# Kernel tuning notes

Hardware: AMD Instinct MI355X
Metric: run time of the kernel (lower is better)

The kernel has to match this reference:

```python
import jax, jax.numpy as jnp
import numpy as np

DIM = 2048
N_HEADS = 16
HEAD_DIM = DIM // N_HEADS
ROPE_BASE = 10000.0


def _rope_cos_sin(seq_len, head_dim, dtype):
    inv_freq = 1.0 / (ROPE_BASE ** (jnp.arange(0, head_dim, 2, dtype=jnp.float32) / head_dim))
    t = jnp.arange(seq_len, dtype=jnp.float32)
    freqs = jnp.einsum('s,d->sd', t, inv_freq)          # (S, hd/2)
    emb = jnp.concatenate([freqs, freqs], axis=-1)       # (S, hd)
    return jnp.cos(emb).astype(dtype), jnp.sin(emb).astype(dtype)


def _rotate_half(x):
    x1, x2 = jnp.split(x, 2, axis=-1)
    return jnp.concatenate([-x2, x1], axis=-1)


def _apply_rope(x, cos, sin):
    # x: (B, H, S, hd); cos/sin: (S, hd)
    return x * cos[None, None] + _rotate_half(x) * sin[None, None]


def setup_inputs() -> dict:
    key = jax.random.key(0)
    ks = jax.random.split(key, 5)
    B, S = 2, 2048
    scale = 1.0 / np.sqrt(DIM)
    return {
        'x': jax.random.normal(ks[0], (B, S, DIM), dtype=jnp.float32),
        'Wq': jax.random.normal(ks[1], (DIM, DIM), dtype=jnp.float32) * scale,
        'Wk': jax.random.normal(ks[2], (DIM, DIM), dtype=jnp.float32) * scale,
        'Wv': jax.random.normal(ks[3], (DIM, DIM), dtype=jnp.float32) * scale,
        'Wo': jax.random.normal(ks[4], (DIM, DIM), dtype=jnp.float32) * scale,
    }


def reference(x, Wq, Wk, Wv, Wo):
    B, S, _ = x.shape
    scale = HEAD_DIM ** -0.5

    def proj(W):
        # torch Linear: x @ W.T ; reshape to (B, H, S, hd)
        return (x @ W.T).reshape(B, S, N_HEADS, HEAD_DIM).transpose(0, 2, 1, 3)

    q, k, v = proj(Wq), proj(Wk), proj(Wv)
    cos, sin = _rope_cos_sin(S, HEAD_DIM, x.dtype)
    q = _apply_rope(q, cos, sin)
    k = _apply_rope(k, cos, sin)

    scores = jnp.einsum('bhqd,bhkd->bhqk', q, k) * scale  # (B,H,S,S)
    causal = jnp.triu(jnp.ones((S, S), dtype=bool), k=1)
    scores = jnp.where(causal[None, None], -jnp.inf, scores)
    attn = jax.nn.softmax(scores.astype(jnp.float32), axis=-1).astype(q.dtype)
    out = jnp.einsum('bhqk,bhkd->bhqd', attn, v)          # (B,H,S,hd)
    out = out.transpose(0, 2, 1, 3).reshape(B, S, DIM)
    return out @ Wo.T
```

## Files before the change

### kernel.cpp

```cpp
#include <hip/hip_runtime.h>


#define SEQ 2048
#define DMODEL 2048
#define NH 16
#define HD 128

typedef __attribute__((ext_vector_type(8))) short bf16x8;
typedef __attribute__((ext_vector_type(4))) float f32x4;

__device__ __forceinline__ unsigned short f2bf(float f) {
  unsigned int u = __float_as_uint(f);
  u += 0x7fffu + ((u >> 16) & 1u);
  return (unsigned short)(u >> 16);
}

__device__ __forceinline__ void g2l16(const void* g, void* l) {
  __builtin_amdgcn_global_load_lds((const __attribute__((address_space(1))) void*)g,
                                   (__attribute__((address_space(3))) void*)l,
                                   16, 0, 0);
}

__device__ __forceinline__ f32x4 mfma16(bf16x8 a, bf16x8 b, f32x4 c) {
  return __builtin_amdgcn_mfma_f32_16x16x32_bf16(a, b, c, 0, 0, 0);
}

template <int CTRL>
__device__ __forceinline__ float dpp_ror(float v) {
  return __int_as_float(__builtin_amdgcn_mov_dpp(__float_as_int(v), CTRL, 0xf, 0xf, false));
}
__device__ __forceinline__ float red_max16(float v) {
  v = fmaxf(v, dpp_ror<0x128>(v));
  v = fmaxf(v, dpp_ror<0x124>(v));
  v = fmaxf(v, dpp_ror<0x122>(v));
  v = fmaxf(v, dpp_ror<0x121>(v));
  return v;
}
__device__ __forceinline__ float red_sum16(float v) {
  v += dpp_ror<0x128>(v);
  v += dpp_ror<0x124>(v);
  v += dpp_ror<0x122>(v);
  v += dpp_ror<0x121>(v);
  return v;
}

__global__ __launch_bounds__(256) void cvt_all(const float* __restrict__ x,
                                               const float* __restrict__ wq,
                                               const float* __restrict__ wk,
                                               const float* __restrict__ wv,
                                               const float* __restrict__ wo,
                                               unsigned short* __restrict__ dst0,
                                               float2* __restrict__ rtab) {
  const int b = blockIdx.x;
  if (b >= 24576) {
    const int idx = (b - 24576) * 256 + threadIdx.x;
    const int s = idx >> 6, d = idx & 63;
    float sn, cs;
    sincosf((float)s * exp2f(-0.20762050593046f * (float)d), &sn, &cs);
    rtab[idx] = make_float2(cs, sn);
    return;
  }
  const float* src;
  unsigned short* dst;
  int idx, r = -1;
  if (b < 8192) {
    src = x; dst = dst0; idx = b * 256 + threadIdx.x;
  } else {
    r = (b - 8192) >> 12;
    src = (r == 0) ? wq : (r == 1) ? wk : (r == 2) ? wv : wo;
    dst = dst0 + (size_t)2 * SEQ * DMODEL + (size_t)r * DMODEL * DMODEL;
    idx = ((b - 8192) & 4095) * 256 + threadIdx.x;
  }
  const float4 v = ((const float4*)src)[idx];
  ushort4 o;
  o.x = f2bf(v.x); o.y = f2bf(v.y); o.z = f2bf(v.z); o.w = f2bf(v.w);
  int widx = idx;
  if (r == 0 || r == 1) {
    const int row = idx >> 9, col = idx & 511;
    const int o_ = row & 127;
    const int e = (((o_ >> 4) & 3) << 5) | (((o_ >> 6) & 1) << 4) | (o_ & 15);
    widx = (((row & ~127) | e) << 9) | col;
  }
  ((ushort4*)dst)[widx] = o;
}

template <int MODE>
__global__ __launch_bounds__(512, 2) void gemm_pipe(
    const unsigned short* __restrict__ A,
    const unsigned short* __restrict__ B,
    unsigned short* __restrict__ obf,
    float* __restrict__ of32,
    const float2* __restrict__ rtab) {
  constexpr int BN = (MODE == 0) ? 192 : 128;
  constexpr int NTW = BN / 32;
  constexpr int TILE = (256 + BN) * 64;
  constexpr int NU = 32 + BN / 8;
  constexpr int UPW = NU / 8;
  __shared__ unsigned short lds[2 * TILE];
  const int nb = blockIdx.x, mb = blockIdx.y;
  const int M0 = mb * 256;
  const int t = threadIdx.x;
  const int w = t >> 6, lane = t & 63, l15 = lane & 15, quad = lane >> 4;
  const int g = lane >> 3, j = lane & 7;
  const int wm = w >> 1, wn = w & 1;

  const unsigned short* Abase = A + (size_t)M0 * DMODEL;
  const unsigned short* Bbase = B + (size_t)nb * BN * DMODEL;

  f32x4 acc[4][NTW] = {};

  auto stage = [&](int buf, int k0, int i0, int i1) {
#pragma unroll
    for (int i = i0; i < i1; ++i) {
      const int u = w * UPW + i;
      if (u < 32) {
        g2l16(Abase + (size_t)(u * 8 + g) * DMODEL + k0 + ((j ^ g) << 3),
              &lds[buf * TILE + u * 512]);
      } else {
        g2l16(Bbase + (size_t)((u - 32) * 8 + g) * DMODEL + k0 + ((j ^ g) << 3),
              &lds[buf * TILE + 16384 + (u - 32) * 512]);
      }
    }
  };

  auto comp = [&](int buf, int kc) {
    const int c = kc * 4 + quad;
    const unsigned short* As_ = &lds[buf * TILE];
    const unsigned short* Bs_ = &lds[buf * TILE + 16384];
    bf16x8 af[4], bv[NTW];
#pragma unroll
    for (int mt = 0; mt < 4; ++mt) {
      const int m = wm * 64 + mt * 16 + l15;
      af[mt] = *(const bf16x8*)&As_[m * 64 + ((c ^ (m & 7)) << 3)];
    }
#pragma unroll
    for (int nt = 0; nt < NTW; ++nt) {
      const int n = wn * (BN / 2) + nt * 16 + l15;
      bv[nt] = *(const bf16x8*)&Bs_[n * 64 + ((c ^ (n & 7)) << 3)];
    }
#pragma unroll
    for (int nt = 0; nt < NTW; ++nt)
#pragma unroll
      for (int mt = 0; mt < 4; ++mt)
        acc[mt][nt] = mfma16(af[mt], bv[nt], acc[mt][nt]);
  };

  stage(0, 0, 0, UPW);
  asm volatile("s_waitcnt vmcnt(0)\n\ts_barrier" ::: "memory");

  int buf = 0;
  for (int tt = 0; tt < 32; ++tt) {
    const bool ps = (tt < 31);
    if (ps) stage(buf ^ 1, tt * 64 + 64, 0, UPW / 2);
    comp(buf, 0);
    if (ps) stage(buf ^ 1, tt * 64 + 64, UPW / 2, UPW);
    comp(buf, 1);
    if (ps) {
      asm volatile("s_waitcnt vmcnt(0)\n\ts_barrier" ::: "memory");
      buf ^= 1;
    }
  }

  if (MODE == 0) {
    const size_t NX = (size_t)2 * SEQ * DMODEL;
#pragma unroll
    for (int pp = 0; pp < NTW / 2; ++pp) {
      const int colb = nb * BN + wn * (BN / 2) + pp * 32;
      const int z = colb >> 11;
      const int zc = colb & 2047;
      const int h = zc >> 7;
      const int e0 = zc & 127;
      if (z < 2) {
        const float qscale = (z == 0) ? 0.1275174356f : 1.0f;
        unsigned short* O = obf + (size_t)z * NX;
        const int rt = (e0 >> 5) * 16 + l15;
#pragma unroll
        for (int mt = 0; mt < 4; ++mt)
#pragma unroll
          for (int reg = 0; reg < 4; ++reg) {
            const int m = M0 + wm * 64 + mt * 16 + quad * 4 + reg;
            const int bb = m >> 11, s = m & 2047;
            unsigned short* ob = O + ((size_t)(bb * NH + h) * SEQ + s) * HD;
            const float2 cs = rtab[s * 64 + rt];
            const float x1 = acc[mt][2 * pp][reg], x2 = acc[mt][2 * pp + 1][reg];
            ob[e0 + l15] = f2bf((x1 * cs.x - x2 * cs.y) * qscale);
            ob[e0 + 16 + l15] = f2bf((x2 * cs.x + x1 * cs.y) * qscale);
          }
      } else {
        unsigned short* Vb0 = obf + 2 * NX + (size_t)h * HD * SEQ;
#pragma unroll
        for (int q2 = 0; q2 < 2; ++q2) {
          const int d = e0 + q2 * 16 + l15;
#pragma unroll
          for (int mt = 0; mt < 4; ++mt)
#pragma unroll
            for (int reg = 0; reg < 4; ++reg) {
              const int m = M0 + wm * 64 + mt * 16 + quad * 4 + reg;
              const int bb = m >> 11, s = m & 2047;
              unsigned short* ob = Vb0 + (size_t)bb * NH * HD * SEQ;
              ob[(size_t)d * SEQ + s] = f2bf(acc[mt][2 * pp + q2][reg]);
            }
        }
      }
    }
  } else {
#pragma unroll
    for (int mt = 0; mt < 4; ++mt)
#pragma unroll
      for (int reg = 0; reg < 4; ++reg) {
        const int m = M0 + wm * 64 + mt * 16 + quad * 4 + reg;
#pragma unroll
        for (int nt = 0; nt < NTW; ++nt)
          of32[(size_t)m * DMODEL + nb * BN + wn * (BN / 2) + nt * 16 + l15] =
              acc[mt][nt][reg];
      }
  }
}

__global__ __launch_bounds__(256) void attn_kernel(const unsigned short* __restrict__ Q,
                                                   const unsigned short* __restrict__ K,
                                                   const unsigned short* __restrict__ Vt,
                                                   unsigned short* __restrict__ Oa) {
  __shared__ unsigned short Ks[2][64 * 128];
  __shared__ unsigned short Vs[2][128 * 64];
  __shared__ unsigned short Ps[4][1024];
  const int gid = blockIdx.x;
  const int bh = gid & 31;
  const int pr = gid >> 5;
  const unsigned short* Qb = Q + (size_t)bh * SEQ * HD;
  const unsigned short* Kb = K + (size_t)bh * SEQ * HD;
  const unsigned short* Vb = Vt + (size_t)bh * HD * SEQ;
  const int t = threadIdx.x;
  const int w = t >> 6, lane = t & 63, l15 = lane & 15, quad = lane >> 4;
  const int l7 = lane & 7;
  const int b = bh >> 4, h = bh & 15;
  const int uA = w * 64 + lane;

  auto stage = [&](int sb, int kt) {
    const unsigned short* Kt = Kb + (size_t)(kt * 64) * HD;
    const unsigned short* Vtk = Vb + kt * 64;
#pragma unroll
    for (int i = 0; i < 4; ++i) {
      const int u = i * 256 + uA;
      const int key = u >> 4, cs = u & 15;
      g2l16(Kt + (size_t)key * HD + ((cs ^ (key & 7)) << 3),
            &Ks[sb][(i * 256 + w * 64) * 8]);
    }
#pragma unroll
    for (int i = 0; i < 4; ++i) {
      const int u = i * 256 + uA;
      const int d = u >> 3, cs = u & 7;
      g2l16(Vtk + (size_t)d * SEQ + ((cs ^ (d & 7)) << 3),
            &Vs[sb][(i * 256 + w * 64) * 8]);
    }
  };

  for (int half = 0; half < 2; ++half) {
    const int qt = half ? 31 - pr : pr;

    bf16x8 qf[4];
#pragma unroll
    for (int ch = 0; ch < 4; ++ch)
      qf[ch] = *(const bf16x8*)(Qb + (size_t)(qt * 64 + w * 16 + l15) * HD +
                                ch * 32 + quad * 8);

    f32x4 o[8] = {};
    float mrow[4], lrow[4];
#pragma unroll
    for (int reg = 0; reg < 4; ++reg) { mrow[reg] = -1e30f; lrow[reg] = 0.f; }

    stage(0, 0);
    asm volatile("s_waitcnt vmcnt(0)\n\ts_barrier" ::: "memory");
    int buf = 0;

    for (int kt = 0; kt <= qt; ++kt) {
      if (kt < qt) stage(buf ^ 1, kt + 1);

      const bool diag = (kt == qt);
      const int ntm = diag ? w : 3;
      f32x4 s[4] = {};
      __builtin_amdgcn_s_setprio(1);
#pragma unroll
      for (int ch = 0; ch < 4; ++ch) {
        const int c = ch * 4 + quad;
#pragma unroll
        for (int nt = 0; nt < 4; ++nt) {
          if (nt <= ntm) {
            const int n = nt * 16 + l15;
            const bf16x8 bv = *(const bf16x8*)&Ks[buf][n * 128 + ((c ^ l7) << 3)];
            s[nt] = mfma16(qf[ch], bv, s[nt]);
          }
        }
      }
      __builtin_amdgcn_s_setprio(0);

      if (diag) {
#pragma unroll
        for (int nt = 0; nt < 4; ++nt)
#pragma unroll
          for (int reg = 0; reg < 4; ++reg) {
            const int rr = w * 16 + quad * 4 + reg;
            const int cc = nt * 16 + l15;
            if (cc > rr) s[nt][reg] = -1e30f;
          }
      }

#pragma unroll
      for (int reg = 0; reg < 4; ++reg) {
        float vmax = s[0][reg];
#pragma unroll
        for (int nt = 1; nt < 4; ++nt) vmax = fmaxf(vmax, s[nt][reg]);
        vmax = red_max16(vmax);
        const float mo = mrow[reg];
        float mn = mo;
        if (!__all(vmax <= mo + 8.0f)) {
          mn = fmaxf(mo, vmax);
          const float alpha = exp2f(mo - mn);
          mrow[reg] = mn;
          lrow[reg] *= alpha;
#pragma unroll
          for (int nt = 0; nt < 8; ++nt) o[nt][reg] *= alpha;
        }
        float rs = 0.f;
#pragma unroll
        for (int nt = 0; nt < 4; ++nt) {
          const float p_ = exp2f(s[nt][reg] - mn);
          s[nt][reg] = p_;
          rs += p_;
        }
        rs = red_sum16(rs);
        lrow[reg] += rs;
      }

      unsigned short* Pw = Ps[w];
#pragma unroll
      for (int nt = 0; nt < 4; ++nt)
#pragma unroll
        for (int reg = 0; reg < 4; ++reg) {
          const int key = nt * 16 + l15;
          Pw[(key >> 3) * 128 + (quad * 4 + reg) * 8 + (key & 7)] = f2bf(s[nt][reg]);
        }

      __builtin_amdgcn_s_setprio(1);
#pragma unroll
      for (int ch2 = 0; ch2 < 2; ++ch2) {
        const int c = ch2 * 4 + quad;
        const bf16x8 pa = *(const bf16x8*)&Pw[c * 128 + l15 * 8];
#pragma unroll
        for (int nt = 0; nt < 8; ++nt) {
          const int d = nt * 16 + l15;
          const bf16x8 vv = *(const bf16x8*)&Vs[buf][d * 64 + ((c ^ l7) << 3)];
          o[nt] = mfma16(pa, vv, o[nt]);
        }
      }
      __builtin_amdgcn_s_setprio(0);

      asm volatile("s_waitcnt vmcnt(0)\n\ts_barrier" ::: "memory");
      buf ^= 1;
    }

#pragma unroll
    for (int reg = 0; reg < 4; ++reg) {
      const int sq = qt * 64 + w * 16 + quad * 4 + reg;
      const float inv_l = 1.0f / lrow[reg];
      unsigned short* ob = Oa + (size_t)(b * SEQ + sq) * DMODEL + h * HD;
#pragma unroll
      for (int nt = 0; nt < 8; ++nt) ob[nt * 16 + l15] = f2bf(o[nt][reg] * inv_l);
    }
  }
}

extern "C" void kernel_launch(void* const* d_in, const int* in_sizes, int n_in,
                              void* d_out, int out_size, void* d_ws, size_t ws_size,
                              hipStream_t stream) {
  const float* x = (const float*)d_in[0];
  const float* Wq = (const float*)d_in[1];
  const float* Wk = (const float*)d_in[2];
  const float* Wv = (const float*)d_in[3];
  const float* Wo = (const float*)d_in[4];
  float* out = (float*)d_out;

  const size_t NX = (size_t)2 * SEQ * DMODEL;
  const size_t NW = (size_t)DMODEL * DMODEL;
  unsigned short* ws = (unsigned short*)d_ws;
  unsigned short* xb = ws;
  unsigned short* wqb = xb + NX;
  unsigned short* wkb = wqb + NW;
  unsigned short* wvb = wkb + NW;
  unsigned short* wob = wvb + NW;
  unsigned short* qb = wob + NW;
  unsigned short* kb = qb + NX;
  unsigned short* vb = kb + NX;
  unsigned short* ab = vb + NX;
  float2* rtab = (float2*)(ab + NX);

  cvt_all<<<25088, 256, 0, stream>>>(x, Wq, Wk, Wv, Wo, ws, rtab);
  gemm_pipe<0><<<dim3(32, 16), 512, 0, stream>>>(xb, wqb, qb, nullptr, rtab);
  attn_kernel<<<512, 256, 0, stream>>>(qb, kb, vb, ab);
  gemm_pipe<1><<<dim3(16, 16), 512, 0, stream>>>(ab, wob, nullptr, out, nullptr);
}
```

Baseline: 356.7 us.

## Use 128-row query tiles with 8 waves per attention block and packed P stores

The attention kernel now gives each 512-thread block a 128-query tile instead of processing two 64-query tiles in turn, so every staged K/V tile is shared by twice as many waves. Work is ordered longest-first, and waves whose rows are fully masked skip the tile. P is written to LDS as packed bf16 pairs through a swizzled layout, and the V projection writes keys in a permuted order so the PV step can read P directly. The cost is a larger block, possible imbalance between waves on diagonal tiles, and more intricate indexing that could hide correctness bugs.

```diff
diff --git a/kernel.cpp b/kernel.cpp
--- a/kernel.cpp
+++ b/kernel.cpp
@@ -197,8 +197,10 @@
             for (int reg = 0; reg < 4; ++reg) {
               const int m = M0 + wm * 64 + mt * 16 + quad * 4 + reg;
               const int bb = m >> 11, s = m & 2047;
+              const int spos = (s & ~63) |
+                               ((mt >> 1) * 32 + quad * 8 + reg * 2 + (mt & 1));
               unsigned short* ob = Vb0 + (size_t)bb * NH * HD * SEQ;
-              ob[(size_t)d * SEQ + s] = f2bf(acc[mt][2 * pp + q2][reg]);
+              ob[(size_t)d * SEQ + spos] = f2bf(acc[mt][2 * pp + q2][reg]);
             }
         }
       }
@@ -217,67 +219,64 @@
   }
 }
 
-__global__ __launch_bounds__(256) void attn_kernel(const unsigned short* __restrict__ Q,
-                                                   const unsigned short* __restrict__ K,
-                                                   const unsigned short* __restrict__ Vt,
-                                                   unsigned short* __restrict__ Oa) {
+__global__ __launch_bounds__(512, 4) void attn_kernel(const unsigned short* __restrict__ Q,
+                                                      const unsigned short* __restrict__ K,
+                                                      const unsigned short* __restrict__ Vt,
+                                                      unsigned short* __restrict__ Oa) {
   __shared__ unsigned short Ks[2][64 * 128];
   __shared__ unsigned short Vs[2][128 * 64];
-  __shared__ unsigned short Ps[4][1024];
+  __shared__ unsigned short Ps[8][1024];
   const int gid = blockIdx.x;
   const int bh = gid & 31;
-  const int pr = gid >> 5;
+  const int qt = 15 - (gid >> 5);
   const unsigned short* Qb = Q + (size_t)bh * SEQ * HD;
   const unsigned short* Kb = K + (size_t)bh * SEQ * HD;
   const unsigned short* Vb = Vt + (size_t)bh * HD * SEQ;
   const int t = threadIdx.x;
   const int w = t >> 6, lane = t & 63, l15 = lane & 15, quad = lane >> 4;
-  const int l7 = lane & 7;
   const int b = bh >> 4, h = bh & 15;
-  const int uA = w * 64 + lane;
 
   auto stage = [&](int sb, int kt) {
     const unsigned short* Kt = Kb + (size_t)(kt * 64) * HD;
     const unsigned short* Vtk = Vb + kt * 64;
 #pragma unroll
-    for (int i = 0; i < 4; ++i) {
-      const int u = i * 256 + uA;
+    for (int i = 0; i < 2; ++i) {
+      const int u = i * 512 + t;
       const int key = u >> 4, cs = u & 15;
       g2l16(Kt + (size_t)key * HD + ((cs ^ (key & 7)) << 3),
-            &Ks[sb][(i * 256 + w * 64) * 8]);
-    }
-#pragma unroll
-    for (int i = 0; i < 4; ++i) {
-      const int u = i * 256 + uA;
+            &Ks[sb][(i * 512 + w * 64) * 8]);
+    }
+#pragma unroll
+    for (int i = 0; i < 2; ++i) {
+      const int u = i * 512 + t;
       const int d = u >> 3, cs = u & 7;
       g2l16(Vtk + (size_t)d * SEQ + ((cs ^ (d & 7)) << 3),
-            &Vs[sb][(i * 256 + w * 64) * 8]);
+            &Vs[sb][(i * 512 + w * 64) * 8]);
     }
   };
 
-  for (int half = 0; half < 2; ++half) {
-    const int qt = half ? 31 - pr : pr;
-
-    bf16x8 qf[4];
-#pragma unroll
-    for (int ch = 0; ch < 4; ++ch)
-      qf[ch] = *(const bf16x8*)(Qb + (size_t)(qt * 64 + w * 16 + l15) * HD +
-                                ch * 32 + quad * 8);
-
-    f32x4 o[8] = {};
-    float mrow[4], lrow[4];
-#pragma unroll
-    for (int reg = 0; reg < 4; ++reg) { mrow[reg] = -1e30f; lrow[reg] = 0.f; }
-
-    stage(0, 0);
-    asm volatile("s_waitcnt vmcnt(0)\n\ts_barrier" ::: "memory");
-    int buf = 0;
-
-    for (int kt = 0; kt <= qt; ++kt) {
-      if (kt < qt) stage(buf ^ 1, kt + 1);
-
-      const bool diag = (kt == qt);
-      const int ntm = diag ? w : 3;
+  bf16x8 qf[4];
+#pragma unroll
+  for (int ch = 0; ch < 4; ++ch)
+    qf[ch] = *(const bf16x8*)(Qb + (size_t)(qt * 128 + w * 16 + l15) * HD +
+                              ch * 32 + quad * 8);
+
+  f32x4 o[8] = {};
+  float mrow[4], lrow[4];
+#pragma unroll
+  for (int reg = 0; reg < 4; ++reg) { mrow[reg] = -1e30f; lrow[reg] = 0.f; }
+
+  const int ktmax = 2 * qt + 1;
+  stage(0, 0);
+  asm volatile("s_waitcnt vmcnt(0)\n\ts_barrier" ::: "memory");
+  int buf = 0;
+
+  for (int kt = 0; kt <= ktmax; ++kt) {
+    if (kt < ktmax) stage(buf ^ 1, kt + 1);
+
+    const int ntm_raw = (qt * 128 + w * 16 + 15 - kt * 64) >> 4;
+    const int ntm = ntm_raw > 3 ? 3 : ntm_raw;
+    if (ntm >= 0) {
       f32x4 s[4] = {};
       __builtin_amdgcn_s_setprio(1);
 #pragma unroll
@@ -287,29 +286,27 @@
         for (int nt = 0; nt < 4; ++nt) {
           if (nt <= ntm) {
             const int n = nt * 16 + l15;
-            const bf16x8 bv = *(const bf16x8*)&Ks[buf][n * 128 + ((c ^ l7) << 3)];
+            const bf16x8 bv = *(const bf16x8*)&Ks[buf][n * 128 + ((c ^ (n & 7)) << 3)];
             s[nt] = mfma16(qf[ch], bv, s[nt]);
           }
         }
       }
       __builtin_amdgcn_s_setprio(0);
 
-      if (diag) {
+      if (kt >= 2 * qt) {
 #pragma unroll
         for (int nt = 0; nt < 4; ++nt)
 #pragma unroll
           for (int reg = 0; reg < 4; ++reg) {
-            const int rr = w * 16 + quad * 4 + reg;
-            const int cc = nt * 16 + l15;
+            const int rr = qt * 128 + w * 16 + quad * 4 + reg;
+            const int cc = kt * 64 + nt * 16 + l15;
             if (cc > rr) s[nt][reg] = -1e30f;
           }
       }
 
 #pragma unroll
       for (int reg = 0; reg < 4; ++reg) {
-        float vmax = s[0][reg];
-#pragma unroll
-        for (int nt = 1; nt < 4; ++nt) vmax = fmaxf(vmax, s[nt][reg]);
+        float vmax = fmaxf(fmaxf(s[0][reg], s[1][reg]), fmaxf(s[2][reg], s[3][reg]));
         vmax = red_max16(vmax);
         const float mo = mrow[reg];
         float mn = mo;
@@ -334,39 +331,50 @@
 
       unsigned short* Pw = Ps[w];
 #pragma unroll
-      for (int nt = 0; nt < 4; ++nt)
+      for (int np = 0; np < 2; ++np)
 #pragma unroll
         for (int reg = 0; reg < 4; ++reg) {
-          const int key = nt * 16 + l15;
-          Pw[(key >> 3) * 128 + (quad * 4 + reg) * 8 + (key & 7)] = f2bf(s[nt][reg]);
-        }
-
+          unsigned int u;
+          asm("v_cvt_pk_bf16_f32 %0, %1, %2"
+              : "=v"(u)
+              : "v"(s[np * 2][reg]), "v"(s[np * 2 + 1][reg]));
+          const int r = quad * 4 + reg;
+          const int ph = ((np ^ (quad & 1)) * 4 + (l15 >> 2) + r) & 7;
+          *(unsigned int*)&Pw[r * 64 + ph * 8 + (l15 & 3) * 2] = u;
+        }
+      asm volatile("" ::: "memory");
+
+      const int ch2max = (ntm >= 2) ? 1 : 0;
       __builtin_amdgcn_s_setprio(1);
 #pragma unroll
       for (int ch2 = 0; ch2 < 2; ++ch2) {
-        const int c = ch2 * 4 + quad;
-        const bf16x8 pa = *(const bf16x8*)&Pw[c * 128 + l15 * 8];
-#pragma unroll
-        for (int nt = 0; nt < 8; ++nt) {
-          const int d = nt * 16 + l15;
-          const bf16x8 vv = *(const bf16x8*)&Vs[buf][d * 64 + ((c ^ l7) << 3)];
-          o[nt] = mfma16(pa, vv, o[nt]);
+        if (ch2 <= ch2max) {
+          const int pnp = ch2 ^ ((l15 >> 2) & 1);
+          const int ph = (pnp * 4 + quad + l15) & 7;
+          const bf16x8 pa = *(const bf16x8*)&Pw[l15 * 64 + ph * 8];
+          const int c = ch2 * 4 + quad;
+#pragma unroll
+          for (int nt = 0; nt < 8; ++nt) {
+            const int d = nt * 16 + l15;
+            const bf16x8 vv = *(const bf16x8*)&Vs[buf][d * 64 + ((c ^ (d & 7)) << 3)];
+            o[nt] = mfma16(pa, vv, o[nt]);
+          }
         }
       }
       __builtin_amdgcn_s_setprio(0);
-
-      asm volatile("s_waitcnt vmcnt(0)\n\ts_barrier" ::: "memory");
-      buf ^= 1;
-    }
-
-#pragma unroll
-    for (int reg = 0; reg < 4; ++reg) {
-      const int sq = qt * 64 + w * 16 + quad * 4 + reg;
-      const float inv_l = 1.0f / lrow[reg];
-      unsigned short* ob = Oa + (size_t)(b * SEQ + sq) * DMODEL + h * HD;
-#pragma unroll
-      for (int nt = 0; nt < 8; ++nt) ob[nt * 16 + l15] = f2bf(o[nt][reg] * inv_l);
-    }
+    }
+
+    asm volatile("s_waitcnt vmcnt(0)\n\ts_barrier" ::: "memory");
+    buf ^= 1;
+  }
+
+#pragma unroll
+  for (int reg = 0; reg < 4; ++reg) {
+    const int sq = qt * 128 + w * 16 + quad * 4 + reg;
+    const float inv_l = 1.0f / lrow[reg];
+    unsigned short* ob = Oa + (size_t)(b * SEQ + sq) * DMODEL + h * HD;
+#pragma unroll
+    for (int nt = 0; nt < 8; ++nt) ob[nt * 16 + l15] = f2bf(o[nt][reg] * inv_l);
   }
 }
 
@@ -396,6 +404,6 @@
 
   cvt_all<<<25088, 256, 0, stream>>>(x, Wq, Wk, Wv, Wo, ws, rtab);
   gemm_pipe<0><<<dim3(32, 16), 512, 0, stream>>>(xb, wqb, qb, nullptr, rtab);
-  attn_kernel<<<512, 256, 0, stream>>>(qb, kb, vb, ab);
+  attn_kernel<<<512, 512, 0, stream>>>(qb, kb, vb, ab);
   gemm_pipe<1><<<dim3(16, 16), 512, 0, stream>>>(ab, wob, nullptr, out, nullptr);
 }
```

After: 362.7 us. About the same (+1.7%).

## Permute V key order to pack P with paired bf16 stores and skip masked PV chunk

Applied to the files above, without the earlier changes.

The V projection epilogue now writes keys within each 64-block in a permuted order that matches the MFMA accumulator layout. The attention kernel can then convert pairs of P values with v_cvt_pk_bf16_f32 and store them as 32-bit swizzled words instead of scalar 16-bit stores. On the diagonal tile it skips the second PV chunk when it is fully masked. This reduces LDS store count and conversion work in the softmax-to-PV handoff, but the permutation has to match exactly between the producer and the consumer.

```diff
diff --git a/kernel.cpp b/kernel.cpp
--- a/kernel.cpp
+++ b/kernel.cpp
@@ -197,8 +197,10 @@
             for (int reg = 0; reg < 4; ++reg) {
               const int m = M0 + wm * 64 + mt * 16 + quad * 4 + reg;
               const int bb = m >> 11, s = m & 2047;
+              const int spos = (s & ~63) |
+                               ((mt >> 1) * 32 + quad * 8 + reg * 2 + (mt & 1));
               unsigned short* ob = Vb0 + (size_t)bb * NH * HD * SEQ;
-              ob[(size_t)d * SEQ + s] = f2bf(acc[mt][2 * pp + q2][reg]);
+              ob[(size_t)d * SEQ + spos] = f2bf(acc[mt][2 * pp + q2][reg]);
             }
         }
       }
@@ -232,7 +234,6 @@
   const unsigned short* Vb = Vt + (size_t)bh * HD * SEQ;
   const int t = threadIdx.x;
   const int w = t >> 6, lane = t & 63, l15 = lane & 15, quad = lane >> 4;
-  const int l7 = lane & 7;
   const int b = bh >> 4, h = bh & 15;
   const int uA = w * 64 + lane;
 
@@ -278,6 +279,7 @@
 
       const bool diag = (kt == qt);
       const int ntm = diag ? w : 3;
+
       f32x4 s[4] = {};
       __builtin_amdgcn_s_setprio(1);
 #pragma unroll
@@ -287,7 +289,7 @@
         for (int nt = 0; nt < 4; ++nt) {
           if (nt <= ntm) {
             const int n = nt * 16 + l15;
-            const bf16x8 bv = *(const bf16x8*)&Ks[buf][n * 128 + ((c ^ l7) << 3)];
+            const bf16x8 bv = *(const bf16x8*)&Ks[buf][n * 128 + ((c ^ (n & 7)) << 3)];
             s[nt] = mfma16(qf[ch], bv, s[nt]);
           }
         }
@@ -307,9 +309,7 @@
 
 #pragma unroll
       for (int reg = 0; reg < 4; ++reg) {
-        float vmax = s[0][reg];
-#pragma unroll
-        for (int nt = 1; nt < 4; ++nt) vmax = fmaxf(vmax, s[nt][reg]);
+        float vmax = fmaxf(fmaxf(s[0][reg], s[1][reg]), fmaxf(s[2][reg], s[3][reg]));
         vmax = red_max16(vmax);
         const float mo = mrow[reg];
         float mn = mo;
@@ -334,23 +334,34 @@
 
       unsigned short* Pw = Ps[w];
 #pragma unroll
-      for (int nt = 0; nt < 4; ++nt)
+      for (int np = 0; np < 2; ++np)
 #pragma unroll
         for (int reg = 0; reg < 4; ++reg) {
-          const int key = nt * 16 + l15;
-          Pw[(key >> 3) * 128 + (quad * 4 + reg) * 8 + (key & 7)] = f2bf(s[nt][reg]);
-        }
-
+          unsigned int u;
+          asm("v_cvt_pk_bf16_f32 %0, %1, %2"
+              : "=v"(u)
+              : "v"(s[np * 2][reg]), "v"(s[np * 2 + 1][reg]));
+          const int r = quad * 4 + reg;
+          const int ph = ((np ^ (quad & 1)) * 4 + (l15 >> 2) + r) & 7;
+          *(unsigned int*)&Pw[r * 64 + ph * 8 + (l15 & 3) * 2] = u;
+        }
+      asm volatile("" ::: "memory");
+
+      const int ch2max = (ntm >= 2) ? 1 : 0;
       __builtin_amdgcn_s_setprio(1);
 #pragma unroll
       for (int ch2 = 0; ch2 < 2; ++ch2) {
-        const int c = ch2 * 4 + quad;
-        const bf16x8 pa = *(const bf16x8*)&Pw[c * 128 + l15 * 8];
-#pragma unroll
-        for (int nt = 0; nt < 8; ++nt) {
-          const int d = nt * 16 + l15;
-          const bf16x8 vv = *(const bf16x8*)&Vs[buf][d * 64 + ((c ^ l7) << 3)];
-          o[nt] = mfma16(pa, vv, o[nt]);
+        if (ch2 <= ch2max) {
+          const int pnp = ch2 ^ ((l15 >> 2) & 1);
+          const int ph = (pnp * 4 + quad + l15) & 7;
+          const bf16x8 pa = *(const bf16x8*)&Pw[l15 * 64 + ph * 8];
+          const int c = ch2 * 4 + quad;
+#pragma unroll
+          for (int nt = 0; nt < 8; ++nt) {
+            const int d = nt * 16 + l15;
+            const bf16x8 vv = *(const bf16x8*)&Vs[buf][d * 64 + ((c ^ (d & 7)) << 3)];
+            o[nt] = mfma16(pa, vv, o[nt]);
+          }
         }
       }
       __builtin_amdgcn_s_setprio(0);
```

Result: no change. 357.4 us (+0.2%).

## Compute transposed scores so each lane owns one query row in attention

Applied to the files above, without the earlier changes.

Swaps the MFMA operands in the QK^T step so each lane holds scores for a single query across keys. This turns the per-row max/sum reductions into lane-local work plus two cross-quad shuffles, and keeps one running max/sum per lane instead of four. P is now packed with v_cvt_pk_bf16_f32 into a swizzled 32-bit LDS layout, and the PV step skips the second key chunk on diagonal tiles where those keys are fully masked. The cost is extra shuffles to broadcast alpha and the normalizer back to the output layout, plus a more complex LDS indexing scheme.

```diff
diff --git a/kernel.cpp b/kernel.cpp
--- a/kernel.cpp
+++ b/kernel.cpp
@@ -23,25 +23,6 @@
 
 __device__ __forceinline__ f32x4 mfma16(bf16x8 a, bf16x8 b, f32x4 c) {
   return __builtin_amdgcn_mfma_f32_16x16x32_bf16(a, b, c, 0, 0, 0);
-}
-
-template <int CTRL>
-__device__ __forceinline__ float dpp_ror(float v) {
-  return __int_as_float(__builtin_amdgcn_mov_dpp(__float_as_int(v), CTRL, 0xf, 0xf, false));
-}
-__device__ __forceinline__ float red_max16(float v) {
-  v = fmaxf(v, dpp_ror<0x128>(v));
-  v = fmaxf(v, dpp_ror<0x124>(v));
-  v = fmaxf(v, dpp_ror<0x122>(v));
-  v = fmaxf(v, dpp_ror<0x121>(v));
-  return v;
-}
-__device__ __forceinline__ float red_sum16(float v) {
-  v += dpp_ror<0x128>(v);
-  v += dpp_ror<0x124>(v);
-  v += dpp_ror<0x122>(v);
-  v += dpp_ror<0x121>(v);
-  return v;
 }
 
 __global__ __launch_bounds__(256) void cvt_all(const float* __restrict__ x,
@@ -232,7 +213,7 @@
   const unsigned short* Vb = Vt + (size_t)bh * HD * SEQ;
   const int t = threadIdx.x;
   const int w = t >> 6, lane = t & 63, l15 = lane & 15, quad = lane >> 4;
-  const int l7 = lane & 7;
+  const int h7 = l15 & 7;
   const int b = bh >> 4, h = bh & 15;
   const int uA = w * 64 + lane;
 
@@ -243,15 +224,13 @@
     for (int i = 0; i < 4; ++i) {
       const int u = i * 256 + uA;
       const int key = u >> 4, cs = u & 15;
-      g2l16(Kt + (size_t)key * HD + ((cs ^ (key & 7)) << 3),
-            &Ks[sb][(i * 256 + w * 64) * 8]);
+      g2l16(Kt + (size_t)key * HD + ((cs ^ (key & 7)) << 3), &Ks[sb][u * 8]);
     }
 #pragma unroll
     for (int i = 0; i < 4; ++i) {
       const int u = i * 256 + uA;
       const int d = u >> 3, cs = u & 7;
-      g2l16(Vtk + (size_t)d * SEQ + ((cs ^ (d & 7)) << 3),
-            &Vs[sb][(i * 256 + w * 64) * 8]);
+      g2l16(Vtk + (size_t)d * SEQ + ((cs ^ (d & 7)) << 3), &Vs[sb][u * 8]);
     }
   };
 
@@ -265,9 +244,7 @@
                                 ch * 32 + quad * 8);
 
     f32x4 o[8] = {};
-    float mrow[4], lrow[4];
-#pragma unroll
-    for (int reg = 0; reg < 4; ++reg) { mrow[reg] = -1e30f; lrow[reg] = 0.f; }
+    float m_ = -1e30f, l_ = 0.f;
 
     stage(0, 0);
     asm volatile("s_waitcnt vmcnt(0)\n\ts_barrier" ::: "memory");
@@ -278,6 +255,7 @@
 
       const bool diag = (kt == qt);
       const int ntm = diag ? w : 3;
+
       f32x4 s[4] = {};
       __builtin_amdgcn_s_setprio(1);
 #pragma unroll
@@ -286,9 +264,9 @@
 #pragma unroll
         for (int nt = 0; nt < 4; ++nt) {
           if (nt <= ntm) {
-            const int n = nt * 16 + l15;
-            const bf16x8 bv = *(const bf16x8*)&Ks[buf][n * 128 + ((c ^ l7) << 3)];
-            s[nt] = mfma16(qf[ch], bv, s[nt]);
+            const int key = nt * 16 + l15;
+            const bf16x8 kf = *(const bf16x8*)&Ks[buf][key * 128 + ((c ^ (key & 7)) << 3)];
+            s[nt] = mfma16(kf, qf[ch], s[nt]);
           }
         }
       }
@@ -299,58 +277,72 @@
         for (int nt = 0; nt < 4; ++nt)
 #pragma unroll
           for (int reg = 0; reg < 4; ++reg) {
-            const int rr = w * 16 + quad * 4 + reg;
-            const int cc = nt * 16 + l15;
-            if (cc > rr) s[nt][reg] = -1e30f;
+            const int key = nt * 16 + quad * 4 + reg;
+            const int qq = w * 16 + l15;
+            if (key > qq) s[nt][reg] = -1e30f;
           }
       }
 
-#pragma unroll
-      for (int reg = 0; reg < 4; ++reg) {
-        float vmax = s[0][reg];
-#pragma unroll
-        for (int nt = 1; nt < 4; ++nt) vmax = fmaxf(vmax, s[nt][reg]);
-        vmax = red_max16(vmax);
-        const float mo = mrow[reg];
-        float mn = mo;
-        if (!__all(vmax <= mo + 8.0f)) {
-          mn = fmaxf(mo, vmax);
-          const float alpha = exp2f(mo - mn);
-          mrow[reg] = mn;
-          lrow[reg] *= alpha;
-#pragma unroll
-          for (int nt = 0; nt < 8; ++nt) o[nt][reg] *= alpha;
-        }
-        float rs = 0.f;
-#pragma unroll
-        for (int nt = 0; nt < 4; ++nt) {
+      float pmax = -1e30f;
+#pragma unroll
+      for (int nt = 0; nt < 4; ++nt)
+        pmax = fmaxf(pmax, fmaxf(fmaxf(s[nt][0], s[nt][1]), fmaxf(s[nt][2], s[nt][3])));
+      pmax = fmaxf(pmax, __shfl_xor(pmax, 16));
+      pmax = fmaxf(pmax, __shfl_xor(pmax, 32));
+      float mn = m_;
+      if (!__all(pmax <= m_ + 8.0f)) {
+        mn = fmaxf(m_, pmax);
+        const float alpha = exp2f(m_ - mn);
+        m_ = mn;
+        l_ *= alpha;
+        float af[4];
+#pragma unroll
+        for (int reg = 0; reg < 4; ++reg) af[reg] = __shfl(alpha, quad * 4 + reg, 16);
+#pragma unroll
+        for (int nt = 0; nt < 8; ++nt)
+#pragma unroll
+          for (int reg = 0; reg < 4; ++reg) o[nt][reg] *= af[reg];
+      }
+      float rs = 0.f;
+#pragma unroll
+      for (int nt = 0; nt < 4; ++nt)
+#pragma unroll
+        for (int reg = 0; reg < 4; ++reg) {
           const float p_ = exp2f(s[nt][reg] - mn);
           s[nt][reg] = p_;
           rs += p_;
         }
-        rs = red_sum16(rs);
-        lrow[reg] += rs;
-      }
-
-      unsigned short* Pw = Ps[w];
+      rs += __shfl_xor(rs, 16);
+      rs += __shfl_xor(rs, 32);
+      l_ += rs;
+
+      unsigned int* Pw32 = (unsigned int*)Ps[w];
 #pragma unroll
       for (int nt = 0; nt < 4; ++nt)
 #pragma unroll
-        for (int reg = 0; reg < 4; ++reg) {
-          const int key = nt * 16 + l15;
-          Pw[(key >> 3) * 128 + (quad * 4 + reg) * 8 + (key & 7)] = f2bf(s[nt][reg]);
-        }
-
+        for (int p = 0; p < 2; ++p) {
+          unsigned int u;
+          asm("v_cvt_pk_bf16_f32 %0, %1, %2"
+              : "=v"(u)
+              : "v"(s[nt][2 * p]), "v"(s[nt][2 * p + 1]));
+          Pw32[l15 * 32 + ((nt * 8 + quad * 2 + p) ^ (h7 << 2))] = u;
+        }
+      asm volatile("" ::: "memory");
+
+      const int ch2max = (ntm >= 2) ? 1 : 0;
       __builtin_amdgcn_s_setprio(1);
 #pragma unroll
       for (int ch2 = 0; ch2 < 2; ++ch2) {
-        const int c = ch2 * 4 + quad;
-        const bf16x8 pa = *(const bf16x8*)&Pw[c * 128 + l15 * 8];
-#pragma unroll
-        for (int nt = 0; nt < 8; ++nt) {
-          const int d = nt * 16 + l15;
-          const bf16x8 vv = *(const bf16x8*)&Vs[buf][d * 64 + ((c ^ l7) << 3)];
-          o[nt] = mfma16(pa, vv, o[nt]);
+        if (ch2 <= ch2max) {
+          const bf16x8 pa =
+              *(const bf16x8*)(Pw32 + l15 * 32 + (((ch2 * 16 + quad * 4) ^ (h7 << 2))));
+          const int c = ch2 * 4 + quad;
+#pragma unroll
+          for (int nt = 0; nt < 8; ++nt) {
+            const int d = nt * 16 + l15;
+            const bf16x8 vv = *(const bf16x8*)&Vs[buf][d * 64 + ((c ^ (d & 7)) << 3)];
+            o[nt] = mfma16(pa, vv, o[nt]);
+          }
         }
       }
       __builtin_amdgcn_s_setprio(0);
@@ -359,13 +351,16 @@
       buf ^= 1;
     }
 
+    float linv[4];
+#pragma unroll
+    for (int reg = 0; reg < 4; ++reg)
+      linv[reg] = 1.0f / __shfl(l_, quad * 4 + reg, 16);
 #pragma unroll
     for (int reg = 0; reg < 4; ++reg) {
       const int sq = qt * 64 + w * 16 + quad * 4 + reg;
-      const float inv_l = 1.0f / lrow[reg];
       unsigned short* ob = Oa + (size_t)(b * SEQ + sq) * DMODEL + h * HD;
 #pragma unroll
-      for (int nt = 0; nt < 8; ++nt) ob[nt * 16 + l15] = f2bf(o[nt][reg] * inv_l);
+      for (int nt = 0; nt < 8; ++nt) ob[nt * 16 + l15] = f2bf(o[nt][reg] * linv[reg]);
     }
   }
 }
```

New measurement: 356.2 us. About the same (-0.1%).
